# Optimization experiments

Hardware: AMD Instinct MI355X
Metric: run time of the kernel (lower is better)

Reference implementation:

```python
import jax, jax.numpy as jnp
import numpy as np

B, S, D, E = 16, 2048, 1024, 524288

def setup_inputs() -> dict:
    key = jax.random.key(0)
    k0, k1, k2, k3 = jax.random.split(key, 4)
    x = jax.random.normal(k0, (B, S, D), dtype=jnp.float32)
    mask = jnp.ones((B, S), dtype=bool)
    edges = jax.random.randint(k1, (2, E), 0, B * S, dtype=jnp.int32)
    scale = 1.0 / np.sqrt(D).astype(np.float32)
    W1 = jax.random.normal(k2, (D, D), dtype=jnp.float32) * scale  # GCNConv lin weight
    b1 = jnp.zeros((D,), dtype=jnp.float32)                        # GCNConv bias
    W2 = jax.random.normal(k3, (D, D), dtype=jnp.float32) * scale  # output Linear
    b2 = jnp.zeros((D,), dtype=jnp.float32)
    return {"x": x, "mask": mask, "edges": edges, "W1": W1, "b1": b1, "W2": W2, "b2": b2}

def reference(x, mask, edges, W1, b1, W2, b2):
    # x: [B,S,D]; mask all-True -> gather == reshape to [N,D]
    N = B * S
    nodes = x.reshape(N, D)
    src, dst = edges[0], edges[1]
    # GCN normalization (gcn_norm, add_self_loops=False): deg over dst, norm = d^-1/2[src]*d^-1/2[dst]
    deg = jax.ops.segment_sum(jnp.ones((E,), dtype=nodes.dtype), dst, num_segments=N)
    dinv = jnp.where(deg > 0, jax.lax.rsqrt(jnp.maximum(deg, 1e-12)), 0.0)
    norm = dinv[src] * dinv[dst]  # [E]
    h = nodes @ W1.T                                   # [N,D] transform
    msg = h[src] * norm[:, None]                       # [E,D] gather + scale
    agg = jax.ops.segment_sum(msg, dst, num_segments=N) + b1  # scatter-aggregate + bias
    g = jax.nn.gelu(agg, approximate=False)            # nn.GELU (exact erf)
    out = g @ W2.T + b2                                # Linear(graph_hid_dim -> input_dim)
    # residual scatter-add back into x (mask all True)
    return x + (out.reshape(B, S, D) * mask[:, :, None].astype(x.dtype))
```

## Files before the change

### kernel.cpp

```cpp
#include <hip/hip_runtime.h>
#include <hip/hip_fp8.h>
#include <stdint.h>

typedef unsigned short u16;
typedef __attribute__((ext_vector_type(8))) short s16x8;
typedef __attribute__((ext_vector_type(4))) float f32x4;
typedef __attribute__((ext_vector_type(2))) float f32x2;

#define D_DIM 1024
#define GK 1024
#define NT 16

__device__ __forceinline__ u16 f2bf(float f) {
  union { float f; uint32_t u; } v; v.f = f;
  uint32_t u = v.u;
  return (u16)((u + 0x7FFFu + ((u >> 16) & 1u)) >> 16);
}
__device__ __forceinline__ float bf2f(u16 b) {
  union { uint32_t u; float f; } v; v.u = ((uint32_t)b) << 16;
  return v.f;
}

__device__ __forceinline__ uint8_t f2fp8(float f) {
#if __has_builtin(__builtin_amdgcn_cvt_pk_fp8_f32)
  int p = __builtin_amdgcn_cvt_pk_fp8_f32(f, f, 0, false);
  return (uint8_t)(p & 0xff);
#else
  return __hip_fp8_e4m3(f).__x;
#endif
}


__device__ __forceinline__ int lds_half_off(int arr, int buf, int half) {
  return ((((arr << 1) | buf) << 1) | half) << 14;
}

__device__ __forceinline__ void stage_half(const u16* __restrict__ g, int rowBase, int kt,
                                           u16* lds, int arr, int buf, int half, int t) {
  const int hoff = lds_half_off(arr, buf, half);
#pragma unroll
  for (int j = 0; j < 2; ++j) {
    const int c = j * 512 + t;
    const int row = c >> 3;
    const int cb = (((c & 7) ^ (row & 7)) << 4);
    const u16* src = g + (size_t)(rowBase + half * 128 + row) * GK + kt * 64 + (cb >> 1);
    __builtin_amdgcn_global_load_lds((const __attribute__((address_space(1))) void*)src,
        (__attribute__((address_space(3))) void*)((char*)lds + hoff + c * 16), 16, 0, 0);
  }
}

template<int QM>
__device__ __forceinline__ void read_sub_a(const u16* lds, int buf, int half, int lane, s16x8* a) {
  const int base = lds_half_off(0, buf, half);
  const int rsel = lane & 15, cb0 = (lane >> 4) << 4;
#pragma unroll
  for (int im = 0; im < 4; ++im) {
    const int row = QM * 64 + im * 16 + rsel;
    const int swz = (row & 7) << 4;
#pragma unroll
    for (int ks = 0; ks < 2; ++ks)
      a[im * 2 + ks] = *(const s16x8*)((const char*)lds + base + row * 128 + ((ks * 64 + cb0) ^ swz));
  }
}

template<int QN>
__device__ __forceinline__ void read_sub_b(const u16* lds, int buf, int half, int rowBase, int lane, s16x8* b) {
  const int base = lds_half_off(1, buf, half);
  const int rsel = lane & 15, cb0 = (lane >> 4) << 4;
#pragma unroll
  for (int in_ = 0; in_ < 2; ++in_) {
    const int row = rowBase + (QN * 2 + in_) * 16 + rsel;
    const int swz = (row & 7) << 4;
#pragma unroll
    for (int ks = 0; ks < 2; ++ks)
      b[in_ * 2 + ks] = *(const s16x8*)((const char*)lds + base + row * 128 + ((ks * 64 + cb0) ^ swz));
  }
}

template<int QM, int QN>
__device__ __forceinline__ void do_quad(f32x4 acc[8][4], const s16x8* aS, const s16x8* bS) {
  __builtin_amdgcn_s_setprio(1);
#pragma unroll
  for (int im = 0; im < 4; ++im)
#pragma unroll
    for (int in_ = 0; in_ < 2; ++in_)
#pragma unroll
      for (int ks = 0; ks < 2; ++ks)
        acc[QM * 4 + im][QN * 2 + in_] = __builtin_amdgcn_mfma_f32_16x16x32_bf16(
            aS[im * 2 + ks], bS[in_ * 2 + ks], acc[QM * 4 + im][QN * 2 + in_], 0, 0, 0);
  __builtin_amdgcn_s_setprio(0);
}

#define BARRIER __builtin_amdgcn_s_barrier()
#define WAIT_LGKM asm volatile("s_waitcnt lgkmcnt(0)" ::: "memory")
#define WAIT_VM(n) asm volatile("s_waitcnt vmcnt(" #n ")" ::: "memory")

template<int EPI>
__global__ __launch_bounds__(512, 2) void gemm256(
    const u16* __restrict__ A, const u16* __restrict__ B, uint8_t* __restrict__ C8,
    const float* __restrict__ bias, const u16* __restrict__ xres, float* __restrict__ Cf)
{
  __shared__ u16 lds[65536];
  const int t = threadIdx.x;
  const int lane = t & 63;
  const int w = t >> 6;
  const int wave_m = w >> 2;
  const int wave_n = w & 3;
  const int halfB = wave_n >> 1;
  const int rowBaseB = (wave_n & 1) * 64;

  const int lb = blockIdx.x;
  const int wid = ((lb & 7) << 6) | (lb >> 3);
  const int bm = wid >> 2;
  const int bn = wid & 3;
  const int rowA = bm * 256;
  const int rowB = bn * 256;

  f32x4 acc[8][4] = {};
  s16x8 aS[8], b0S[4], b1S[4];

  stage_half(A, rowA, 0, lds, 0, 0, 0, t);
  stage_half(A, rowA, 0, lds, 0, 0, 1, t);
  stage_half(B, rowB, 0, lds, 1, 0, 0, t);
  stage_half(B, rowB, 0, lds, 1, 0, 1, t);
  stage_half(B, rowB, 1, lds, 1, 1, 0, t);
  stage_half(B, rowB, 1, lds, 1, 1, 1, t);
  WAIT_VM(4);
  BARRIER;

  for (int i = 0; i < NT / 2 - 1; ++i) {
    const int t1 = 2 * i + 1;
    read_sub_a<0>(lds, 0, wave_m, lane, aS);
    read_sub_b<0>(lds, 0, halfB, rowBaseB, lane, b0S);
    stage_half(A, rowA, t1, lds, 0, 1, 0, t);
    BARRIER; WAIT_LGKM;
    do_quad<0, 0>(acc, aS, b0S);
    BARRIER;
    read_sub_b<1>(lds, 0, halfB, rowBaseB, lane, b1S);
    stage_half(A, rowA, t1, lds, 0, 1, 1, t);
    BARRIER; WAIT_LGKM;
    do_quad<0, 1>(acc, aS, b1S);
    BARRIER;
    read_sub_a<1>(lds, 0, wave_m, lane, aS);
    stage_half(B, rowB, 2 * i + 2, lds, 1, 0, 0, t);
    BARRIER; WAIT_LGKM;
    do_quad<1, 1>(acc, aS, b1S);
    BARRIER;
    stage_half(B, rowB, 2 * i + 2, lds, 1, 0, 1, t);
    WAIT_VM(4);
    BARRIER;
    do_quad<1, 0>(acc, aS, b0S);
    BARRIER;
    read_sub_a<0>(lds, 1, wave_m, lane, aS);
    read_sub_b<0>(lds, 1, halfB, rowBaseB, lane, b0S);
    stage_half(A, rowA, 2 * i + 2, lds, 0, 0, 0, t);
    BARRIER; WAIT_LGKM;
    do_quad<0, 0>(acc, aS, b0S);
    BARRIER;
    read_sub_b<1>(lds, 1, halfB, rowBaseB, lane, b1S);
    stage_half(A, rowA, 2 * i + 2, lds, 0, 0, 1, t);
    BARRIER; WAIT_LGKM;
    do_quad<0, 1>(acc, aS, b1S);
    BARRIER;
    read_sub_a<1>(lds, 1, wave_m, lane, aS);
    stage_half(B, rowB, 2 * i + 3, lds, 1, 1, 0, t);
    BARRIER; WAIT_LGKM;
    do_quad<1, 1>(acc, aS, b1S);
    BARRIER;
    stage_half(B, rowB, 2 * i + 3, lds, 1, 1, 1, t);
    WAIT_VM(4);
    BARRIER;
    do_quad<1, 0>(acc, aS, b0S);
    BARRIER;
  }

  {
    read_sub_a<0>(lds, 0, wave_m, lane, aS);
    read_sub_b<0>(lds, 0, halfB, rowBaseB, lane, b0S);
    stage_half(A, rowA, NT - 1, lds, 0, 1, 0, t);
    BARRIER; WAIT_LGKM;
    do_quad<0, 0>(acc, aS, b0S);
    BARRIER;
    read_sub_b<1>(lds, 0, halfB, rowBaseB, lane, b1S);
    stage_half(A, rowA, NT - 1, lds, 0, 1, 1, t);
    BARRIER; WAIT_LGKM;
    do_quad<0, 1>(acc, aS, b1S);
    BARRIER;
    read_sub_a<1>(lds, 0, wave_m, lane, aS);
    BARRIER; WAIT_LGKM;
    do_quad<1, 1>(acc, aS, b1S);
    BARRIER;
    WAIT_VM(0);
    BARRIER;
    do_quad<1, 0>(acc, aS, b0S);
    read_sub_a<0>(lds, 1, wave_m, lane, aS);
    read_sub_b<0>(lds, 1, halfB, rowBaseB, lane, b0S);
    WAIT_LGKM;
    do_quad<0, 0>(acc, aS, b0S);
    read_sub_b<1>(lds, 1, halfB, rowBaseB, lane, b1S);
    WAIT_LGKM;
    do_quad<0, 1>(acc, aS, b1S);
    read_sub_a<1>(lds, 1, wave_m, lane, aS);
    WAIT_LGKM;
    do_quad<1, 1>(acc, aS, b1S);
    do_quad<1, 0>(acc, aS, b0S);
  }

  const int row0 = rowA + wave_m * 128 + ((lane >> 4) << 2);
  const int col0 = rowB + wave_n * 64 + (lane & 15);
  if (EPI == 0) {
#pragma unroll
    for (int mf = 0; mf < 8; ++mf)
#pragma unroll
      for (int nf = 0; nf < 4; ++nf) {
        const int c = col0 + nf * 16;
#pragma unroll
        for (int r = 0; r < 4; ++r)
          C8[(size_t)(row0 + mf * 16 + r) * D_DIM + c] = f2fp8(acc[mf][nf][r]);
      }
  } else {
#pragma unroll
    for (int mf = 0; mf < 8; ++mf)
#pragma unroll
      for (int nf = 0; nf < 4; ++nf) {
        const int c = col0 + nf * 16;
        const float bv = bias[c];
#pragma unroll
        for (int r = 0; r < 4; ++r) {
          const size_t idx = (size_t)(row0 + mf * 16 + r) * D_DIM + c;
          Cf[idx] = acc[mf][nf][r] + bv + bf2f(xres[idx]);
        }
      }
  }
}

__global__ void cast_f32_bf16(const float* __restrict__ in, u16* __restrict__ out, long n) {
  long i = ((long)blockIdx.x * blockDim.x + threadIdx.x) * 4;
  if (i >= n) return;
  const float4 v = *(const float4*)(in + i);
  ushort4 o;
  o.x = f2bf(v.x); o.y = f2bf(v.y); o.z = f2bf(v.z); o.w = f2bf(v.w);
  *(ushort4*)(out + i) = o;
}

__global__ void deg_count_int(const int* __restrict__ dst, int* __restrict__ cnt, int E) {
  int i = blockIdx.x * blockDim.x + threadIdx.x;
  if (i < E) atomicAdd(&cnt[dst[i]], 1);
}

__global__ __launch_bounds__(1024) void scan_offsets(const int* __restrict__ cnt,
                                                     int* __restrict__ off,
                                                     int* __restrict__ cursor,
                                                     float* __restrict__ dinv, int N) {
  __shared__ int part[1024];
  const int t = threadIdx.x;
  const int nper = (N + 1023) / 1024;
  const int base = t * nper;
  int s = 0;
  for (int i = 0; i < nper; ++i) {
    int idx = base + i;
    if (idx < N) s += cnt[idx];
  }
  part[t] = s;
  __syncthreads();
  for (int d = 1; d < 1024; d <<= 1) {
    int v = (t >= d) ? part[t - d] : 0;
    __syncthreads();
    part[t] += v;
    __syncthreads();
  }
  int run = (t > 0) ? part[t - 1] : 0;
  for (int i = 0; i < nper; ++i) {
    int idx = base + i;
    if (idx < N) {
      const int c = cnt[idx];
      off[idx] = run;
      cursor[idx] = run;
      dinv[idx] = c > 0 ? rsqrtf((float)c) : 0.f;
      run += c;
    }
  }
  if (t == 1023) off[N] = run;
}

__global__ void fill_csr(const int* __restrict__ src, const int* __restrict__ dst,
                         const float* __restrict__ dinv, int* __restrict__ cursor,
                         uint2* __restrict__ ebuf, int E) {
  int e = blockIdx.x * blockDim.x + threadIdx.x;
  if (e >= E) return;
  const int d = dst[e], s = src[e];
  const int pos = atomicAdd(&cursor[d], 1);
  const float nrm = dinv[s] * dinv[d];
  uint2 en; en.x = (unsigned)s; en.y = __float_as_uint(nrm);
  ebuf[pos] = en;
}

__device__ __forceinline__ void acc8_fp8(float* a, uint2 hv, float nrm) {
#if __has_builtin(__builtin_amdgcn_cvt_pk_f32_fp8)
  const f32x2 p0 = __builtin_amdgcn_cvt_pk_f32_fp8(hv.x, false);
  const f32x2 p1 = __builtin_amdgcn_cvt_pk_f32_fp8(hv.x, true);
  const f32x2 p2 = __builtin_amdgcn_cvt_pk_f32_fp8(hv.y, false);
  const f32x2 p3 = __builtin_amdgcn_cvt_pk_f32_fp8(hv.y, true);
  a[0] += p0.x * nrm; a[1] += p0.y * nrm;
  a[2] += p1.x * nrm; a[3] += p1.y * nrm;
  a[4] += p2.x * nrm; a[5] += p2.y * nrm;
  a[6] += p3.x * nrm; a[7] += p3.y * nrm;
#else
  const float s = nrm * 0x1p+120f;
#pragma unroll
  for (int k = 0; k < 8; ++k) {
    const uint32_t word = (k < 4) ? hv.x : hv.y;
    const uint32_t b = (word >> ((k & 3) * 8)) & 0xffu;
    a[k] += __uint_as_float(((b & 0x80u) << 24) | ((b & 0x7fu) << 20)) * s;
  }
#endif
}

__device__ __forceinline__ float gelu_exact(float t) {
  return 0.5f * t * (1.0f + erff(t * 0.70710678118f));
}

__global__ __launch_bounds__(256) void aggregate_gelu_fp8(
    const uint8_t* __restrict__ h8, const uint2* __restrict__ ebuf,
    const int* __restrict__ off, const float* __restrict__ b1,
    u16* __restrict__ g)
{
  const int node = __builtin_amdgcn_readfirstlane(blockIdx.x * 2 + (threadIdx.x >> 7));
  const int lt = threadIdx.x & 127;
  const int fb = lt * 8;
  const int beg = off[node], end = off[node + 1];
  float a[8] = {0.f, 0.f, 0.f, 0.f, 0.f, 0.f, 0.f, 0.f};

  int i = beg;
  for (; i + 2 <= end; i += 2) {
    const uint2 ea = ebuf[i];
    const uint2 eb = ebuf[i + 1];
    const uint2 ha = *(const uint2*)(h8 + (size_t)ea.x * D_DIM + fb);
    const uint2 hb = *(const uint2*)(h8 + (size_t)eb.x * D_DIM + fb);
    acc8_fp8(a, ha, __uint_as_float(ea.y));
    acc8_fp8(a, hb, __uint_as_float(eb.y));
  }
  if (i < end) {
    const uint2 ea = ebuf[i];
    const uint2 ha = *(const uint2*)(h8 + (size_t)ea.x * D_DIM + fb);
    acc8_fp8(a, ha, __uint_as_float(ea.y));
  }

  const float4 bA = *(const float4*)(b1 + fb);
  const float4 bB = *(const float4*)(b1 + fb + 4);
  const float v0 = gelu_exact(a[0] + bA.x), v1 = gelu_exact(a[1] + bA.y);
  const float v2 = gelu_exact(a[2] + bA.z), v3 = gelu_exact(a[3] + bA.w);
  const float v4 = gelu_exact(a[4] + bB.x), v5 = gelu_exact(a[5] + bB.y);
  const float v6 = gelu_exact(a[6] + bB.z), v7 = gelu_exact(a[7] + bB.w);
  uint4 o;
  o.x = (uint32_t)f2bf(v0) | ((uint32_t)f2bf(v1) << 16);
  o.y = (uint32_t)f2bf(v2) | ((uint32_t)f2bf(v3) << 16);
  o.z = (uint32_t)f2bf(v4) | ((uint32_t)f2bf(v5) << 16);
  o.w = (uint32_t)f2bf(v6) | ((uint32_t)f2bf(v7) << 16);
  *(uint4*)(g + (size_t)node * D_DIM + fb) = o;
}

extern "C" void kernel_launch(void* const* d_in, const int* in_sizes, int n_in,
                              void* d_out, int out_size, void* d_ws, size_t ws_size,
                              hipStream_t stream) {
  const float* x  = (const float*)d_in[0];
  const int* edges = (const int*)d_in[2];
  const float* W1 = (const float*)d_in[3];
  const float* b1 = (const float*)d_in[4];
  const float* W2 = (const float*)d_in[5];
  const float* b2 = (const float*)d_in[6];
  float* out = (float*)d_out;

  const int D = D_DIM;
  const long ND = (long)in_sizes[0];
  const int N = (int)(ND / D);
  const int E = in_sizes[2] / 2;
  const int* src = edges;
  const int* dst = edges + E;

  u16* xbf    = (u16*)d_ws;
  u16* gbf    = xbf + ND;
  uint8_t* h8 = (uint8_t*)(gbf + ND);
  u16* w1b    = (u16*)(h8 + ND);
  u16* w2b    = w1b + (size_t)D * D;
  int* cnt    = (int*)(w2b + (size_t)D * D);
  int* off    = cnt + N;
  int* cursor = off + N + 1;
  float* dnv  = (float*)(cursor + N);
  uint2* ebuf = (uint2*)(dnv + N + 1);

  hipMemsetAsync(cnt, 0, (size_t)N * sizeof(int), stream);

  cast_f32_bf16<<<(int)(ND / 4 / 256), 256, 0, stream>>>(x, xbf, ND);
  cast_f32_bf16<<<(int)((long)D * D / 4 / 256), 256, 0, stream>>>(W1, w1b, (long)D * D);
  cast_f32_bf16<<<(int)((long)D * D / 4 / 256), 256, 0, stream>>>(W2, w2b, (long)D * D);

  deg_count_int<<<(E + 255) / 256, 256, 0, stream>>>(dst, cnt, E);
  scan_offsets<<<1, 1024, 0, stream>>>(cnt, off, cursor, dnv, N);
  fill_csr<<<(E + 255) / 256, 256, 0, stream>>>(src, dst, dnv, cursor, ebuf, E);

  gemm256<0><<<(N / 256) * (D / 256), 512, 0, stream>>>(xbf, w1b, h8, nullptr, nullptr, nullptr);

  aggregate_gelu_fp8<<<N / 2, 256, 0, stream>>>(h8, ebuf, off, b1, gbf);

  gemm256<1><<<(N / 256) * (D / 256), 512, 0, stream>>>(gbf, w2b, nullptr, b2, xbf, out);
}
```

Measured before the change: 437.5 us.

## Stage fp8 GEMM epilogue through LDS, merge cast kernels, unroll aggregation by four

The first GEMM's fp8 output is now written into LDS per wave and then stored to global memory as 16-byte rows, replacing scattered single-byte stores. The three f32-to-bf16 cast launches become one grid-stride kernel, which removes two launches. The aggregation loop is unrolled from two to four edges so more gathers are in flight at once. The LDS staging adds a barrier and requires the LDS buffer to be large enough to give each wave 8 KB.

```diff
diff --git a/kernel.cpp b/kernel.cpp
--- a/kernel.cpp
+++ b/kernel.cpp
@@ -206,19 +206,28 @@
     do_quad<1, 0>(acc, aS, b0S);
   }
 
-  const int row0 = rowA + wave_m * 128 + ((lane >> 4) << 2);
-  const int col0 = rowB + wave_n * 64 + (lane & 15);
   if (EPI == 0) {
+    BARRIER;
+    uint8_t* lb8 = (uint8_t*)lds + w * 8192;
 #pragma unroll
     for (int mf = 0; mf < 8; ++mf)
 #pragma unroll
-      for (int nf = 0; nf < 4; ++nf) {
-        const int c = col0 + nf * 16;
+      for (int nf = 0; nf < 4; ++nf)
 #pragma unroll
         for (int r = 0; r < 4; ++r)
-          C8[(size_t)(row0 + mf * 16 + r) * D_DIM + c] = f2fp8(acc[mf][nf][r]);
-      }
+          lb8[(mf * 16 + ((lane >> 4) << 2) + r) * 64 + nf * 16 + (lane & 15)] =
+              f2fp8(acc[mf][nf][r]);
+    const size_t rowG = (size_t)(rowA + wave_m * 128);
+    const int colG = rowB + wave_n * 64;
+#pragma unroll
+    for (int s = 0; s < 8; ++s) {
+      const uint4 v = *(const uint4*)(lb8 + s * 1024 + lane * 16);
+      const size_t row = rowG + s * 16 + (lane >> 2);
+      *(uint4*)(C8 + row * D_DIM + colG + (lane & 3) * 16) = v;
+    }
   } else {
+    const int row0 = rowA + wave_m * 128 + ((lane >> 4) << 2);
+    const int col0 = rowB + wave_n * 64 + (lane & 15);
 #pragma unroll
     for (int mf = 0; mf < 8; ++mf)
 #pragma unroll
@@ -234,13 +243,21 @@
   }
 }
 
-__global__ void cast_f32_bf16(const float* __restrict__ in, u16* __restrict__ out, long n) {
-  long i = ((long)blockIdx.x * blockDim.x + threadIdx.x) * 4;
-  if (i >= n) return;
-  const float4 v = *(const float4*)(in + i);
-  ushort4 o;
-  o.x = f2bf(v.x); o.y = f2bf(v.y); o.z = f2bf(v.z); o.w = f2bf(v.w);
-  *(ushort4*)(out + i) = o;
+__global__ void cast_all_bf16(const float* __restrict__ x, u16* __restrict__ xb, long nx4,
+                              const float* __restrict__ w1, u16* __restrict__ w1b,
+                              const float* __restrict__ w2, u16* __restrict__ w2b, long nw4) {
+  const long total = nx4 + 2 * nw4;
+  for (long i = (long)blockIdx.x * blockDim.x + threadIdx.x; i < total;
+       i += (long)gridDim.x * blockDim.x) {
+    const float* in; u16* out; long j;
+    if (i < nx4) { in = x; out = xb; j = i; }
+    else if (i < nx4 + nw4) { in = w1; out = w1b; j = i - nx4; }
+    else { in = w2; out = w2b; j = i - nx4 - nw4; }
+    const float4 v = *(const float4*)(in + j * 4);
+    ushort4 o;
+    o.x = f2bf(v.x); o.y = f2bf(v.y); o.z = f2bf(v.z); o.w = f2bf(v.w);
+    *(ushort4*)(out + j * 4) = o;
+  }
 }
 
 __global__ void deg_count_int(const int* __restrict__ dst, int* __restrict__ cnt, int E) {
@@ -332,15 +349,18 @@
   float a[8] = {0.f, 0.f, 0.f, 0.f, 0.f, 0.f, 0.f, 0.f};
 
   int i = beg;
-  for (; i + 2 <= end; i += 2) {
-    const uint2 ea = ebuf[i];
-    const uint2 eb = ebuf[i + 1];
-    const uint2 ha = *(const uint2*)(h8 + (size_t)ea.x * D_DIM + fb);
-    const uint2 hb = *(const uint2*)(h8 + (size_t)eb.x * D_DIM + fb);
-    acc8_fp8(a, ha, __uint_as_float(ea.y));
-    acc8_fp8(a, hb, __uint_as_float(eb.y));
-  }
-  if (i < end) {
+  for (; i + 4 <= end; i += 4) {
+    const uint2 e0 = ebuf[i], e1 = ebuf[i + 1], e2 = ebuf[i + 2], e3 = ebuf[i + 3];
+    const uint2 h0 = *(const uint2*)(h8 + (size_t)e0.x * D_DIM + fb);
+    const uint2 h1 = *(const uint2*)(h8 + (size_t)e1.x * D_DIM + fb);
+    const uint2 h2 = *(const uint2*)(h8 + (size_t)e2.x * D_DIM + fb);
+    const uint2 h3 = *(const uint2*)(h8 + (size_t)e3.x * D_DIM + fb);
+    acc8_fp8(a, h0, __uint_as_float(e0.y));
+    acc8_fp8(a, h1, __uint_as_float(e1.y));
+    acc8_fp8(a, h2, __uint_as_float(e2.y));
+    acc8_fp8(a, h3, __uint_as_float(e3.y));
+  }
+  for (; i < end; ++i) {
     const uint2 ea = ebuf[i];
     const uint2 ha = *(const uint2*)(h8 + (size_t)ea.x * D_DIM + fb);
     acc8_fp8(a, ha, __uint_as_float(ea.y));
@@ -391,9 +411,7 @@
 
   hipMemsetAsync(cnt, 0, (size_t)N * sizeof(int), stream);
 
-  cast_f32_bf16<<<(int)(ND / 4 / 256), 256, 0, stream>>>(x, xbf, ND);
-  cast_f32_bf16<<<(int)((long)D * D / 4 / 256), 256, 0, stream>>>(W1, w1b, (long)D * D);
-  cast_f32_bf16<<<(int)((long)D * D / 4 / 256), 256, 0, stream>>>(W2, w2b, (long)D * D);
+  cast_all_bf16<<<2048, 256, 0, stream>>>(x, xbf, ND / 4, W1, w1b, W2, w2b, (long)D * D / 4);
 
   deg_count_int<<<(E + 255) / 256, 256, 0, stream>>>(dst, cnt, E);
   scan_offsets<<<1, 1024, 0, stream>>>(cnt, off, cursor, dnv, N);
```

New measurement: 435.8 us. Within noise of the previous version (-0.4%).
